# Kernel optimization log

Hardware: AMD Instinct MI355X
Metric: run time of the kernel (lower is better)

Reference implementation:

```python
import jax, jax.numpy as jnp
import numpy as np

N, M, P, C_IN, C_OUT = 100000, 50000, 1600000, 128, 128
NEG_SLOPE = 0.2


def segment_softmax(w, seg, num):
    # numerically-stable softmax of w over segments defined by seg
    m = jax.ops.segment_max(w, seg, num_segments=num)
    e = jnp.exp(w - m[seg])
    s = jax.ops.segment_sum(e, seg, num_segments=num)
    return e / s[seg]


def setup_inputs() -> dict:
    key = jax.random.key(0)
    ks = jax.random.split(key, 8)
    scale = 1.0 / np.sqrt(C_IN)
    return {
        "X": jax.random.normal(ks[0], (N, C_IN), dtype=jnp.float32),
        "pair_v": jax.random.randint(ks[1], (P,), 0, N, dtype=jnp.int32),
        "pair_e": jax.random.randint(ks[2], (P,), 0, M, dtype=jnp.int32),
        "src_v": jax.random.randint(ks[3], (P,), 0, N, dtype=jnp.int32),
        "W_theta": jax.random.normal(ks[4], (C_OUT, C_IN), dtype=jnp.float32) * scale,
        "b_theta": jax.random.normal(ks[5], (C_OUT,), dtype=jnp.float32) * scale,
        "w_src": jax.random.normal(ks[6], (C_OUT,), dtype=jnp.float32) * scale,
        "w_dst": jax.random.normal(ks[7], (C_OUT,), dtype=jnp.float32) * scale,
    }


def reference(X, pair_v, pair_e, src_v, W_theta, b_theta, w_src, w_dst):
    # theta: linear projection (eval mode: dropout = identity, no BN)
    H = X @ W_theta.T + b_theta                      # [N, C_OUT]

    # per-pair attention scores: atten_src(H)[src] + atten_dst(H)[dst]
    s = H @ w_src                                    # [N]
    d = H @ w_dst                                    # [N]
    score = jax.nn.leaky_relu(s[src_v] + d[pair_v], NEG_SLOPE)  # [P]
    score = jnp.clip(score, 0.001, 5.0)

    # degrees
    ones = jnp.ones((P,), dtype=H.dtype)
    de = jnp.maximum(jax.ops.segment_sum(ones, pair_e, num_segments=M), 1.0)  # [M]
    dv = jnp.maximum(jax.ops.segment_sum(ones, pair_v, num_segments=N), 1.0)  # [N]

    dv_isqrt = dv ** -0.5
    Xs = H * dv_isqrt[:, None]
    Xe = jax.ops.segment_sum(Xs[pair_v], pair_e, num_segments=M) / de[:, None]  # [M, C]
    Hs = jax.ops.segment_sum(Xe[pair_e], pair_v, num_segments=N) * dv_isqrt[:, None]

    # v2v(aggr='softmax_then_sum', e2v_weight=score):
    #   v2e softmax_then_sum with unit weights == per-edge mean
    Xe1 = jax.ops.segment_sum(Hs[pair_v], pair_e, num_segments=M) / de[:, None]
    #   e2v: segment-softmax the scores per destination vertex, weighted sum
    alpha = segment_softmax(score, pair_v, N)        # [P]
    Xv1 = jax.ops.segment_sum(alpha[:, None] * Xe1[pair_e], pair_v, num_segments=N)

    # v2v(aggr='mean', v2e_aggr='softmax_then_sum'):
    #   v2e softmax_then_sum with unit weights == per-edge mean; e2v mean
    Xe2 = jax.ops.segment_sum(Xv1[pair_v], pair_e, num_segments=M) / de[:, None]
    Xv2 = jax.ops.segment_sum(Xe2[pair_e], pair_v, num_segments=N) / dv[:, None]

    # is_last=False: ELU activation (dropout identity in eval)
    return jax.nn.elu(Xv2)
```

## Files before the change

kernel.cpp:

```cpp
#include <hip/hip_runtime.h>
#include <math.h>

#define M_EDGES 50000
#define CHUNK 1024

#define NBMAX 200
#define TILE_E 4096
#define TILE_V 4096
#define CAPL_E 44
#define CAPL_V 32

typedef unsigned int u32;
typedef unsigned short u16;
typedef float f32x4 __attribute__((ext_vector_type(4)));
typedef short bf16x8 __attribute__((ext_vector_type(8)));

__device__ __forceinline__ float bflo(u32 u) { return __uint_as_float(u << 16); }
__device__ __forceinline__ float bfhi(u32 u) { return __uint_as_float(u & 0xffff0000u); }
__device__ __forceinline__ u32 packbf(float x, float y) {
  u32 a = __float_as_uint(x); a += 0x7fffu + ((a >> 16) & 1u);
  u32 b = __float_as_uint(y); b += 0x7fffu + ((b >> 16) & 1u);
  return (a >> 16) | (b & 0xffff0000u);
}
__device__ __forceinline__ u32 bf16rne(float x) {
  u32 a = __float_as_uint(x);
  a += 0x7fffu + ((a >> 16) & 1u);
  return a >> 16;
}
__device__ __forceinline__ void bfsplit(float f, u32& h, u32& l) {
  h = bf16rne(f);
  const float hf = __uint_as_float(h << 16);
  l = bf16rne(f - hf);
}

__global__ __launch_bounds__(256) void bin_edge_kernel(
    const int* __restrict__ pair_e, const int* __restrict__ pair_v,
    u32* __restrict__ out, int* __restrict__ gcur,
    int P, int SE, int NB) {
  __shared__ int lcnt[NBMAX];
  __shared__ int gbase[NBMAX];
  __shared__ u32 stage[NBMAX][CAPL_E];
  const int tid = (int)threadIdx.x;
  const int p0 = blockIdx.x * TILE_E;
  const int pend = (p0 + TILE_E < P) ? p0 + TILE_E : P;
  const u32 maskE = (1u << SE) - 1u;
  for (int b = tid; b < NB; b += 256) lcnt[b] = 0;
  __syncthreads();
  for (int p = p0 + tid; p < pend; p += 256) {
    const int e = pair_e[p];
    const int v = pair_v[p];
    const int b = e >> SE;
    const u32 entry = (u32)v | (((u32)e & maskE) << 17);
    const int pos = atomicAdd(&lcnt[b], 1);
    if (pos < CAPL_E) stage[b][pos] = entry;
    else out[atomicAdd(&gcur[b], 1)] = entry;
  }
  __syncthreads();
  for (int b = tid; b < NB; b += 256) {
    const int n = lcnt[b] < CAPL_E ? lcnt[b] : CAPL_E;
    gbase[b] = atomicAdd(&gcur[b], n);
  }
  __syncthreads();
  const int wv = tid >> 6, lane = tid & 63;
  for (int b = wv; b < NB; b += 4) {
    const int n = lcnt[b] < CAPL_E ? lcnt[b] : CAPL_E;
    if (lane < n) out[gbase[b] + lane] = stage[b][lane];
  }
}

__global__ __launch_bounds__(256) void bin_vtx_kernel(
    const int* __restrict__ pair_e, const int* __restrict__ pair_v,
    const int* __restrict__ src_v,
    uint2* __restrict__ out, int* __restrict__ gcur,
    int P, int SV, int NB) {
  __shared__ int lcnt[NBMAX];
  __shared__ int gbase[NBMAX];
  __shared__ uint2 stage[NBMAX][CAPL_V];
  const int tid = (int)threadIdx.x;
  const int p0 = blockIdx.x * TILE_V;
  const int pend = (p0 + TILE_V < P) ? p0 + TILE_V : P;
  const u32 maskV = (1u << SV) - 1u;
  for (int b = tid; b < NB; b += 256) lcnt[b] = 0;
  __syncthreads();
  for (int p = p0 + tid; p < pend; p += 256) {
    const int e = pair_e[p];
    const int v = pair_v[p];
    const int s = src_v[p];
    const int b = v >> SV;
    uint2 entry;
    entry.x = ((u32)v & maskV) | ((u32)e << SV);
    entry.y = (u32)s;
    const int pos = atomicAdd(&lcnt[b], 1);
    if (pos < CAPL_V) stage[b][pos] = entry;
    else out[atomicAdd(&gcur[b], 1)] = entry;
  }
  __syncthreads();
  for (int b = tid; b < NB; b += 256) {
    const int n = lcnt[b] < CAPL_V ? lcnt[b] : CAPL_V;
    gbase[b] = atomicAdd(&gcur[b], n);
  }
  __syncthreads();
  const int wv = tid >> 6, lane = tid & 63;
  for (int b = wv; b < NB; b += 4) {
    const int n = lcnt[b] < CAPL_V ? lcnt[b] : CAPL_V;
    if (lane < n) out[gbase[b] + lane] = stage[b][lane];
  }
}

__global__ void init_gcur_kernel(int* __restrict__ ge, int* __restrict__ gv,
                                 int NBE, int NBV, int capgE, int capgV) {
  const int t = (int)threadIdx.x;
  if (t < NBE) ge[t] = t * capgE;
  if (t < NBV) gv[t] = t * capgV;
}

__global__ __launch_bounds__(256) void bucket_hist_kernel(
    const u32* __restrict__ entE, const int* __restrict__ gcurE, int* __restrict__ cnt_e,
    const uint2* __restrict__ entV, const int* __restrict__ gcurV, int* __restrict__ cnt_v,
    int NBE, int SE, int capgE, int SV, int capgV, int M, int N) {
  __shared__ int h[1024];
  const int b = (int)blockIdx.x;
  const int tid = (int)threadIdx.x;
  if (b < NBE) {
    const int nb = 1 << SE;
    for (int t = tid; t < nb; t += 256) h[t] = 0;
    __syncthreads();
    const int end = gcurE[b];
    for (int i = b * capgE + tid; i < end; i += 256)
      atomicAdd(&h[entE[i] >> 17], 1);
    __syncthreads();
    const int base = b << SE;
    for (int t = tid; t < nb; t += 256)
      if (base + t < M) cnt_e[base + t] = h[t];
  } else {
    const int bb = b - NBE;
    const int nb = 1 << SV;
    for (int t = tid; t < nb; t += 256) h[t] = 0;
    __syncthreads();
    const int end = gcurV[bb];
    const u32 mask = (1u << SV) - 1u;
    for (int i = bb * capgV + tid; i < end; i += 256)
      atomicAdd(&h[entV[i].x & mask], 1);
    __syncthreads();
    const int base = bb << SV;
    for (int t = tid; t < nb; t += 256)
      if (base + t < N) cnt_v[base + t] = h[t];
  }
}

__global__ __launch_bounds__(512) void unbin_edge_kernel(
    const u32* __restrict__ ent, const int* __restrict__ gcur,
    int* __restrict__ cur_e, int* __restrict__ edge_vtx,
    int SE, int capg) {
  const int b = blockIdx.x;
  const int end = gcur[b];
  const int ebase = b << SE;
  for (int i = b * capg + (int)threadIdx.x; i < end; i += 512) {
    const u32 w = ent[i];
    const int v = (int)(w & 0x1ffffu);
    const int e = ebase + (int)(w >> 17);
    edge_vtx[atomicAdd(&cur_e[e], 1)] = v;
  }
}

__global__ __launch_bounds__(512) void unbin_vtx_kernel(
    const uint2* __restrict__ ent, const int* __restrict__ gcur,
    int* __restrict__ cur_v, int2* __restrict__ vtx_es, int* __restrict__ vtx_edge,
    const float* __restrict__ svec, const float* __restrict__ dvec,
    int SV, int capg) {
  const int b = blockIdx.x;
  const int end = gcur[b];
  const int vbase = b << SV;
  const u32 maskV = (1u << SV) - 1u;
  for (int i = b * capg + (int)threadIdx.x; i < end; i += 512) {
    const uint2 w = ent[i];
    const int v = vbase + (int)(w.x & maskV);
    const int e = (int)(w.x >> SV);
    float sc = svec[w.y] + dvec[v];
    sc = sc > 0.f ? sc : 0.2f * sc;
    sc = fminf(fmaxf(sc, 0.001f), 5.0f);
    const int iv = atomicAdd(&cur_v[v], 1);
    vtx_es[iv] = make_int2(e, __float_as_int(__expf(sc)));
    vtx_edge[iv] = e;
  }
}

__global__ __launch_bounds__(1024) void blocksum_kernel(
    const int* __restrict__ cnt_e, const int* __restrict__ cnt_v,
    int* __restrict__ part, int CE, int M, int N) {
  const int b = blockIdx.x;
  const int* cnt;
  int n, chunk;
  if (b < CE) { cnt = cnt_e; n = M; chunk = b; }
  else        { cnt = cnt_v; n = N; chunk = b - CE; }
  const int i = chunk * CHUNK + (int)threadIdx.x;
  int x = (i < n) ? cnt[i] : 0;
#pragma unroll
  for (int m = 32; m >= 1; m >>= 1) x += __shfl_xor(x, m, 64);
  __shared__ int ws[16];
  if ((threadIdx.x & 63) == 0) ws[threadIdx.x >> 6] = x;
  __syncthreads();
  if (threadIdx.x == 0) {
    int t = 0;
#pragma unroll
    for (int q = 0; q < 16; ++q) t += ws[q];
    part[b] = t;
  }
}

__global__ __launch_bounds__(256) void partscan_kernel(
    int* __restrict__ part, int CE, int CV,
    int* __restrict__ off_e, int* __restrict__ off_v, int M, int N) {
  __shared__ int sh[256];
  const int tid = (int)threadIdx.x;
  for (int s = 0; s < 2; ++s) {
    const int base = s ? CE : 0;
    const int count = s ? CV : CE;
    int x = (tid < count) ? part[base + tid] : 0;
    sh[tid] = x;
    __syncthreads();
    for (int ofs = 1; ofs < 256; ofs <<= 1) {
      int v = (tid >= ofs) ? sh[tid - ofs] : 0;
      __syncthreads();
      sh[tid] += v;
      __syncthreads();
    }
    if (tid < count) part[base + tid] = sh[tid] - x;
    if (tid == 0) {
      const int tot = sh[count - 1];
      if (s == 0) off_e[M] = tot; else off_v[N] = tot;
    }
    __syncthreads();
  }
}

__global__ __launch_bounds__(1024) void blockscan_kernel(
    const int* __restrict__ cnt_e, const int* __restrict__ cnt_v,
    const int* __restrict__ part,
    int* __restrict__ off_e, int* __restrict__ off_v,
    int* __restrict__ cur_e, int* __restrict__ cur_v,
    float* __restrict__ de_inv, float* __restrict__ dv_inv, float* __restrict__ dv_isqrt,
    int CE, int M, int N) {
  __shared__ int sh[CHUNK];
  const int b = blockIdx.x;
  const int tid = (int)threadIdx.x;
  const int* cnt;
  int n, chunk;
  int *off, *cur;
  float *i1, *i2;
  if (b < CE) { cnt = cnt_e; n = M; chunk = b;      off = off_e; cur = cur_e; i1 = de_inv; i2 = nullptr; }
  else        { cnt = cnt_v; n = N; chunk = b - CE; off = off_v; cur = cur_v; i1 = dv_inv; i2 = dv_isqrt; }
  const int i = chunk * CHUNK + tid;
  const int x = (i < n) ? cnt[i] : 0;
  sh[tid] = x;
  __syncthreads();
  for (int ofs = 1; ofs < CHUNK; ofs <<= 1) {
    int v = (tid >= ofs) ? sh[tid - ofs] : 0;
    __syncthreads();
    sh[tid] += v;
    __syncthreads();
  }
  if (i < n) {
    const int o = part[b] + sh[tid] - x;
    off[i] = o;
    cur[i] = o;
    const float m = (float)(x > 1 ? x : 1);
    i1[i] = 1.0f / m;
    if (i2) i2[i] = 1.0f / sqrtf(m);
  }
}

__global__ __launch_bounds__(256) void prep_w_kernel(
    const float* __restrict__ W, u16* __restrict__ whi, u16* __restrict__ wlo) {
  const int i = (int)blockIdx.x * 256 + (int)threadIdx.x;
  if (i >= 128 * 128) return;
  u32 h, l;
  bfsplit(W[i], h, l);
  whi[i] = (u16)h;
  wlo[i] = (u16)l;
}

#define XPAD 136
__global__ __launch_bounds__(256) void gemm_mfma_kernel(
    const float* __restrict__ X,
    const u16* __restrict__ whi, const u16* __restrict__ wlo,
    const float* __restrict__ bias, const float* __restrict__ wsrc,
    const float* __restrict__ wdst, const float* __restrict__ dv_isqrt,
    u16* __restrict__ Hb, float* __restrict__ s_out, float* __restrict__ d_out,
    int N) {
  __shared__ u16 xhi[64 * XPAD];
  __shared__ u16 xlo[64 * XPAD];
  __shared__ float sred[64];
  __shared__ float dred[64];
  const int tid = (int)threadIdx.x;
  const int row0 = (int)blockIdx.x * 64;

  if (tid < 64) { sred[tid] = 0.f; dred[tid] = 0.f; }
  for (int g = tid; g < 64 * 32; g += 256) {
    const int r = g >> 5;
    const int k4 = (g & 31) << 2;
    int rr = row0 + r; if (rr >= N) rr = N - 1;
    const float4 v = *(const float4*)(X + (size_t)rr * 128 + k4);
    u32 h0, l0, h1, l1, h2, l2, h3, l3;
    bfsplit(v.x, h0, l0); bfsplit(v.y, h1, l1);
    bfsplit(v.z, h2, l2); bfsplit(v.w, h3, l3);
    *(uint2*)(xhi + r * XPAD + k4) = make_uint2(h0 | (h1 << 16), h2 | (h3 << 16));
    *(uint2*)(xlo + r * XPAD + k4) = make_uint2(l0 | (l1 << 16), l2 | (l3 << 16));
  }
  __syncthreads();

  const int wv = tid >> 6;
  const int l  = tid & 63;
  const int lr = l & 15;
  const int lg = l >> 4;
  const int cb = wv * 32;

  f32x4 zero = {0.f, 0.f, 0.f, 0.f};
  f32x4 acc[4][2];
#pragma unroll
  for (int rt = 0; rt < 4; ++rt) { acc[rt][0] = zero; acc[rt][1] = zero; }

#pragma unroll
  for (int kk = 0; kk < 4; ++kk) {
    const int kof = kk * 32 + lg * 8;
    const bf16x8 bh0 = *(const bf16x8*)(whi + (size_t)(cb + lr) * 128 + kof);
    const bf16x8 bh1 = *(const bf16x8*)(whi + (size_t)(cb + 16 + lr) * 128 + kof);
    const bf16x8 bl0 = *(const bf16x8*)(wlo + (size_t)(cb + lr) * 128 + kof);
    const bf16x8 bl1 = *(const bf16x8*)(wlo + (size_t)(cb + 16 + lr) * 128 + kof);
#pragma unroll
    for (int rt = 0; rt < 4; ++rt) {
      const bf16x8 ah = *(const bf16x8*)(xhi + (rt * 16 + lr) * XPAD + kof);
      const bf16x8 al = *(const bf16x8*)(xlo + (rt * 16 + lr) * XPAD + kof);
      acc[rt][0] = __builtin_amdgcn_mfma_f32_16x16x32_bf16(ah, bh0, acc[rt][0], 0, 0, 0);
      acc[rt][1] = __builtin_amdgcn_mfma_f32_16x16x32_bf16(ah, bh1, acc[rt][1], 0, 0, 0);
      acc[rt][0] = __builtin_amdgcn_mfma_f32_16x16x32_bf16(al, bh0, acc[rt][0], 0, 0, 0);
      acc[rt][1] = __builtin_amdgcn_mfma_f32_16x16x32_bf16(al, bh1, acc[rt][1], 0, 0, 0);
      acc[rt][0] = __builtin_amdgcn_mfma_f32_16x16x32_bf16(ah, bl0, acc[rt][0], 0, 0, 0);
      acc[rt][1] = __builtin_amdgcn_mfma_f32_16x16x32_bf16(ah, bl1, acc[rt][1], 0, 0, 0);
    }
  }

  const int c0 = cb + lr, c1 = cb + 16 + lr;
  const float bb0 = bias[c0], bb1 = bias[c1];
  const float ws0 = wsrc[c0], ws1 = wsrc[c1];
  const float wd0 = wdst[c0], wd1 = wdst[c1];
#pragma unroll
  for (int rt = 0; rt < 4; ++rt) {
#pragma unroll
    for (int j = 0; j < 4; ++j) {
      const int rl = rt * 16 + lg * 4 + j;
      const int row = row0 + rl;
      const float h0 = acc[rt][0][j] + bb0;
      const float h1 = acc[rt][1][j] + bb1;
      float sp = h0 * ws0 + h1 * ws1;
      float dp = h0 * wd0 + h1 * wd1;
#pragma unroll
      for (int m = 1; m <= 8; m <<= 1) {
        sp += __shfl_xor(sp, m, 64);
        dp += __shfl_xor(dp, m, 64);
      }
      if (lr == 0) { atomicAdd(&sred[rl], sp); atomicAdd(&dred[rl], dp); }
      if (row < N) {
        const float sc = dv_isqrt[row];
        Hb[(size_t)row * 128 + c0] = (u16)bf16rne(h0 * sc);
        Hb[(size_t)row * 128 + c1] = (u16)bf16rne(h1 * sc);
      }
    }
  }
  __syncthreads();
  if (tid < 64) {
    const int row = row0 + tid;
    if (row < N) { s_out[row] = sred[tid]; d_out[row] = dred[tid]; }
  }
}

#define ACC8(r, p)                                         \
  a[0] += bflo((r).x) * (p); a[1] += bfhi((r).x) * (p);    \
  a[2] += bflo((r).y) * (p); a[3] += bfhi((r).y) * (p);    \
  a[4] += bflo((r).z) * (p); a[5] += bfhi((r).z) * (p);    \
  a[6] += bflo((r).w) * (p); a[7] += bfhi((r).w) * (p);

__global__ __launch_bounds__(256) void seg_pass_kernel(
    const u16* __restrict__ src, u16* __restrict__ dst,
    const int* __restrict__ off, const int* __restrict__ lst,
    const float* __restrict__ post_scale, int nseg) {
  const int seg = blockIdx.x * 4 + ((int)threadIdx.x >> 6);
  if (seg >= nseg) return;
  const int lane = (int)threadIdx.x & 63;
  const int q = lane >> 4;
  const int cl = lane & 15;
  const int beg = off[seg], end = off[seg + 1];
  const int last = end - 1;
  float a[8] = {};
  for (int t0 = beg + q; t0 < end; t0 += 32) {
    int jj[8];
    float ww[8];
    jj[0] = lst[t0];
    ww[0] = 1.f;
#pragma unroll
    for (int u = 1; u < 8; ++u) {
      const int t = t0 + 4 * u;
      jj[u] = lst[t <= last ? t : last];
      ww[u] = t <= last ? 1.f : 0.f;
    }
    uint4 rr[8];
#pragma unroll
    for (int u = 0; u < 8; ++u)
      rr[u] = *(const uint4*)(src + (size_t)jj[u] * 128 + cl * 8);
#pragma unroll
    for (int u = 0; u < 8; ++u) {
      const uint4 r = rr[u];
      const float p = ww[u];
      ACC8(r, p)
    }
  }
#pragma unroll
  for (int k = 0; k < 8; ++k) {
    a[k] += __shfl_xor(a[k], 16, 64);
    a[k] += __shfl_xor(a[k], 32, 64);
  }
  if (q != 0) return;
  const float ps = post_scale[seg];
  uint4 pk;
  pk.x = packbf(a[0] * ps, a[1] * ps); pk.y = packbf(a[2] * ps, a[3] * ps);
  pk.z = packbf(a[4] * ps, a[5] * ps); pk.w = packbf(a[6] * ps, a[7] * ps);
  *(uint4*)(dst + (size_t)seg * 128 + cl * 8) = pk;
}

__global__ __launch_bounds__(256) void segn_pass_kernel(
    const u16* __restrict__ src, void* __restrict__ dst,
    const int* __restrict__ off, const int* __restrict__ lst,
    const float* __restrict__ post_scale, int nseg, int final_mode) {
  const int seg = blockIdx.x * 4 + ((int)threadIdx.x >> 6);
  if (seg >= nseg) return;
  const int lane = (int)threadIdx.x & 63;
  const int q = lane >> 4;
  const int cl = lane & 15;
  const int beg = off[seg], end = off[seg + 1];
  const int last = end - 1;
  float a[8] = {};
  for (int t0 = beg + q; t0 < end; t0 += 16) {
    const int t1 = t0 + 4, t2 = t0 + 8, t3 = t0 + 12;
    const int j0 = lst[t0];
    const int j1 = lst[t1 <= last ? t1 : last];
    const int j2 = lst[t2 <= last ? t2 : last];
    const int j3 = lst[t3 <= last ? t3 : last];
    const float w1 = t1 <= last ? 1.f : 0.f;
    const float w2 = t2 <= last ? 1.f : 0.f;
    const float w3 = t3 <= last ? 1.f : 0.f;
    const uint4 r0 = *(const uint4*)(src + (size_t)j0 * 128 + cl * 8);
    const uint4 r1 = *(const uint4*)(src + (size_t)j1 * 128 + cl * 8);
    const uint4 r2 = *(const uint4*)(src + (size_t)j2 * 128 + cl * 8);
    const uint4 r3 = *(const uint4*)(src + (size_t)j3 * 128 + cl * 8);
    ACC8(r0, 1.0f) ACC8(r1, w1) ACC8(r2, w2) ACC8(r3, w3)
  }
#pragma unroll
  for (int k = 0; k < 8; ++k) {
    a[k] += __shfl_xor(a[k], 16, 64);
    a[k] += __shfl_xor(a[k], 32, 64);
  }
  if (q != 0) return;
  const float ps = post_scale[seg];
#pragma unroll
  for (int k = 0; k < 8; ++k) a[k] *= ps;
  if (final_mode) {
#pragma unroll
    for (int k = 0; k < 8; ++k) a[k] = a[k] > 0.f ? a[k] : __expf(a[k]) - 1.0f;
    float* o = (float*)dst + (size_t)seg * 128 + cl * 8;
    f32x4 v0 = {a[0], a[1], a[2], a[3]};
    f32x4 v1 = {a[4], a[5], a[6], a[7]};
    __builtin_nontemporal_store(v0, (f32x4*)o);
    __builtin_nontemporal_store(v1, (f32x4*)(o + 4));
  } else {
    uint4 pk;
    pk.x = packbf(a[0], a[1]); pk.y = packbf(a[2], a[3]);
    pk.z = packbf(a[4], a[5]); pk.w = packbf(a[6], a[7]);
    *(uint4*)((u16*)dst + (size_t)seg * 128 + cl * 8) = pk;
  }
}

__global__ __launch_bounds__(256) void attn_pass_kernel(
    const u16* __restrict__ src, u16* __restrict__ dst,
    const int* __restrict__ off, const int2* __restrict__ lst_es, int nseg) {
  const int seg = blockIdx.x * 4 + ((int)threadIdx.x >> 6);
  if (seg >= nseg) return;
  const int lane = (int)threadIdx.x & 63;
  const int q = lane >> 4;
  const int cl = lane & 15;
  const int beg = off[seg], end = off[seg + 1];
  const int last = end - 1;
  float a[8] = {};
  float den = 0.f;
  for (int t0 = beg + q; t0 < end; t0 += 16) {
    const int t1 = t0 + 4, t2 = t0 + 8, t3 = t0 + 12;
    const int2 e0 = lst_es[t0];
    const int2 e1 = lst_es[t1 <= last ? t1 : last];
    const int2 e2 = lst_es[t2 <= last ? t2 : last];
    const int2 e3 = lst_es[t3 <= last ? t3 : last];
    const float s0 = __int_as_float(e0.y);
    const float s1 = t1 <= last ? __int_as_float(e1.y) : 0.f;
    const float s2 = t2 <= last ? __int_as_float(e2.y) : 0.f;
    const float s3 = t3 <= last ? __int_as_float(e3.y) : 0.f;
    const uint4 r0 = *(const uint4*)(src + (size_t)e0.x * 128 + cl * 8);
    const uint4 r1 = *(const uint4*)(src + (size_t)e1.x * 128 + cl * 8);
    const uint4 r2 = *(const uint4*)(src + (size_t)e2.x * 128 + cl * 8);
    const uint4 r3 = *(const uint4*)(src + (size_t)e3.x * 128 + cl * 8);
    ACC8(r0, s0) ACC8(r1, s1) ACC8(r2, s2) ACC8(r3, s3)
    den += s0 + s1 + s2 + s3;
  }
#pragma unroll
  for (int k = 0; k < 8; ++k) {
    a[k] += __shfl_xor(a[k], 16, 64);
    a[k] += __shfl_xor(a[k], 32, 64);
  }
  den += __shfl_xor(den, 16, 64);
  den += __shfl_xor(den, 32, 64);
  const float inv = (end > beg) ? 1.0f / den : 0.0f;
  if (q != 0) return;
  uint4 pk;
  pk.x = packbf(a[0] * inv, a[1] * inv); pk.y = packbf(a[2] * inv, a[3] * inv);
  pk.z = packbf(a[4] * inv, a[5] * inv); pk.w = packbf(a[6] * inv, a[7] * inv);
  *(uint4*)(dst + (size_t)seg * 128 + cl * 8) = pk;
}

extern "C" void kernel_launch(void* const* d_in, const int* in_sizes, int n_in,
                              void* d_out, int out_size, void* d_ws, size_t ws_size,
                              hipStream_t stream) {
  const float* X      = (const float*)d_in[0];
  const int*   pair_v = (const int*)d_in[1];
  const int*   pair_e = (const int*)d_in[2];
  const int*   src_v  = (const int*)d_in[3];
  const float* W      = (const float*)d_in[4];
  const float* bias   = (const float*)d_in[5];
  const float* wsrc   = (const float*)d_in[6];
  const float* wdst   = (const float*)d_in[7];

  const int N = in_sizes[0] / 128;
  const int P = in_sizes[1];
  const int M = M_EDGES;
  const int CE = (M + CHUNK - 1) / CHUNK;
  const int CV = (N + CHUNK - 1) / CHUNK;

  int SE = 8;
  while ((((M - 1) >> SE) + 1) > NBMAX) ++SE;
  const int NBE = ((M - 1) >> SE) + 1;
  int SV = 9;
  while ((((N - 1) >> SV) + 1) > NBMAX) ++SV;
  const int NBV = ((N - 1) >> SV) + 1;
  const int capgE = P / NBE + P / (NBE * 8) + 256;
  const int capgV = P / NBV + P / (NBV * 8) + 256;

  char* w = (char*)d_ws;
  auto alloc = [&](size_t bytes) -> char* {
    char* p = w;
    w += (bytes + 255) & ~(size_t)255;
    return p;
  };
  int*   cnt_e     = (int*)alloc((size_t)M * 4);
  int*   cnt_v     = (int*)alloc((size_t)N * 4);
  int*   cur_e     = (int*)alloc((size_t)M * 4);
  int*   cur_v     = (int*)alloc((size_t)N * 4);
  int*   part      = (int*)alloc((size_t)(CE + CV) * 4);
  int*   edge_off  = (int*)alloc((size_t)(M + 1) * 4);
  int*   vtx_off   = (int*)alloc((size_t)(N + 1) * 4);
  float* de_inv    = (float*)alloc((size_t)M * 4);
  float* dv_inv    = (float*)alloc((size_t)N * 4);
  float* dv_isqrt  = (float*)alloc((size_t)N * 4);
  float* svec      = (float*)alloc((size_t)N * 4);
  float* dvec      = (float*)alloc((size_t)N * 4);
  int*   edge_vtx  = (int*)alloc((size_t)P * 4);
  int2*  vtx_es    = (int2*)alloc((size_t)P * 8);
  int*   vtx_edge  = (int*)alloc((size_t)P * 4);
  u16*   bufN      = (u16*)alloc((size_t)N * 128 * 2);
  u16*   bufM      = (u16*)alloc((size_t)M * 128 * 2);
  u32*   binE      = (u32*)alloc((size_t)NBE * capgE * 4);
  uint2* binV      = (uint2*)alloc((size_t)NBV * capgV * 8);
  int*   gcur_e    = (int*)alloc((size_t)NBE * 4);
  int*   gcur_v    = (int*)alloc((size_t)NBV * 4);
  u16*   whi_g     = (u16*)alloc((size_t)128 * 128 * 2);
  u16*   wlo_g     = (u16*)alloc((size_t)128 * 128 * 2);

  prep_w_kernel<<<64, 256, 0, stream>>>(W, whi_g, wlo_g);
  init_gcur_kernel<<<1, 256, 0, stream>>>(gcur_e, gcur_v, NBE, NBV, capgE, capgV);
  bin_edge_kernel<<<(P + TILE_E - 1) / TILE_E, 256, 0, stream>>>(
      pair_e, pair_v, binE, gcur_e, P, SE, NBE);
  bin_vtx_kernel<<<(P + TILE_V - 1) / TILE_V, 256, 0, stream>>>(
      pair_e, pair_v, src_v, binV, gcur_v, P, SV, NBV);
  bucket_hist_kernel<<<NBE + NBV, 256, 0, stream>>>(
      binE, gcur_e, cnt_e, binV, gcur_v, cnt_v, NBE, SE, capgE, SV, capgV, M, N);
  blocksum_kernel<<<CE + CV, 1024, 0, stream>>>(cnt_e, cnt_v, part, CE, M, N);
  partscan_kernel<<<1, 256, 0, stream>>>(part, CE, CV, edge_off, vtx_off, M, N);
  blockscan_kernel<<<CE + CV, 1024, 0, stream>>>(cnt_e, cnt_v, part, edge_off, vtx_off,
                                                 cur_e, cur_v, de_inv, dv_inv, dv_isqrt,
                                                 CE, M, N);
  gemm_mfma_kernel<<<(N + 63) / 64, 256, 0, stream>>>(X, whi_g, wlo_g, bias, wsrc, wdst,
                                                      dv_isqrt, bufN, svec, dvec, N);
  unbin_edge_kernel<<<NBE, 512, 0, stream>>>(binE, gcur_e, cur_e, edge_vtx, SE, capgE);
  unbin_vtx_kernel<<<NBV, 512, 0, stream>>>(binV, gcur_v, cur_v, vtx_es, vtx_edge,
                                            svec, dvec, SV, capgV);

  const int gm = (M + 3) / 4;
  const int gn = (N + 3) / 4;
  seg_pass_kernel<<<gm, 256, 0, stream>>>(bufN, bufM, edge_off, edge_vtx, de_inv, M);
  segn_pass_kernel<<<gn, 256, 0, stream>>>(bufM, bufN, vtx_off, vtx_edge, dv_isqrt, N, 0);
  seg_pass_kernel<<<gm, 256, 0, stream>>>(bufN, bufM, edge_off, edge_vtx, de_inv, M);
  attn_pass_kernel<<<gn, 256, 0, stream>>>(bufM, bufN, vtx_off, vtx_es, N);
  seg_pass_kernel<<<gm, 256, 0, stream>>>(bufN, bufM, edge_off, edge_vtx, de_inv, M);
  segn_pass_kernel<<<gn, 256, 0, stream>>>(bufM, d_out, vtx_off, vtx_edge, dv_inv, N, 1);
}
```

Baseline: 617.2 us.

## Stage CSR scatter in shared memory with LDS cursors during unbinning

The unbin kernels now keep per-segment write cursors in shared memory and place entries into a shared-memory staging buffer. Each block then writes its contiguous CSR slice to global memory in a coalesced pass. This removes the global atomics on cur_e/cur_v and the random global scatter writes, and drops the cur arrays from the scan kernel. The vertex kernel processes its bin in two halves, so it reads the bin entries twice. Large LDS use (about 38-49KB) limits occupancy, and entries beyond the stage capacity fall back to direct global writes.

```diff
diff --git a/kernel.cpp b/kernel.cpp
--- a/kernel.cpp
+++ b/kernel.cpp
@@ -9,6 +9,8 @@
 #define TILE_V 4096
 #define CAPL_E 44
 #define CAPL_V 32
+#define STAGEE 9472
+#define STAGEV 5888
 
 typedef unsigned int u32;
 typedef unsigned short u16;
@@ -150,38 +152,83 @@
 
 __global__ __launch_bounds__(512) void unbin_edge_kernel(
     const u32* __restrict__ ent, const int* __restrict__ gcur,
-    int* __restrict__ cur_e, int* __restrict__ edge_vtx,
-    int SE, int capg) {
+    const int* __restrict__ off_e, int* __restrict__ edge_vtx,
+    int SE, int capg, int M) {
+  __shared__ int stage[STAGEE];
+  __shared__ int ecur[512];
   const int b = blockIdx.x;
+  const int tid = (int)threadIdx.x;
+  const int ebase = b << SE;
+  const int ne = 1 << SE;
+  const int elim = (ebase + ne < M) ? ebase + ne : M;
+  const int sbeg = off_e[ebase];
+  const int send = off_e[elim];
+  for (int t = tid; t < ne; t += 512)
+    ecur[t] = ((ebase + t) < M ? off_e[ebase + t] : send) - sbeg;
+  __syncthreads();
   const int end = gcur[b];
-  const int ebase = b << SE;
-  for (int i = b * capg + (int)threadIdx.x; i < end; i += 512) {
+  for (int i = b * capg + tid; i < end; i += 512) {
     const u32 w = ent[i];
     const int v = (int)(w & 0x1ffffu);
-    const int e = ebase + (int)(w >> 17);
-    edge_vtx[atomicAdd(&cur_e[e], 1)] = v;
-  }
+    const int le = (int)(w >> 17);
+    const int pos = atomicAdd(&ecur[le], 1);
+    if (pos < STAGEE) stage[pos] = v;
+    else edge_vtx[sbeg + pos] = v;
+  }
+  __syncthreads();
+  const int len = send - sbeg;
+  const int lim = len < STAGEE ? len : STAGEE;
+  for (int i = tid; i < lim; i += 512)
+    edge_vtx[sbeg + i] = stage[i];
 }
 
 __global__ __launch_bounds__(512) void unbin_vtx_kernel(
     const uint2* __restrict__ ent, const int* __restrict__ gcur,
-    int* __restrict__ cur_v, int2* __restrict__ vtx_es, int* __restrict__ vtx_edge,
+    const int* __restrict__ off_v, int2* __restrict__ vtx_es, int* __restrict__ vtx_edge,
     const float* __restrict__ svec, const float* __restrict__ dvec,
-    int SV, int capg) {
+    int SV, int capg, int N) {
+  __shared__ int2 stage[STAGEV];
+  __shared__ int vcur[512];
   const int b = blockIdx.x;
-  const int end = gcur[b];
+  const int tid = (int)threadIdx.x;
   const int vbase = b << SV;
   const u32 maskV = (1u << SV) - 1u;
-  for (int i = b * capg + (int)threadIdx.x; i < end; i += 512) {
-    const uint2 w = ent[i];
-    const int v = vbase + (int)(w.x & maskV);
-    const int e = (int)(w.x >> SV);
-    float sc = svec[w.y] + dvec[v];
-    sc = sc > 0.f ? sc : 0.2f * sc;
-    sc = fminf(fmaxf(sc, 0.001f), 5.0f);
-    const int iv = atomicAdd(&cur_v[v], 1);
-    vtx_es[iv] = make_int2(e, __float_as_int(__expf(sc)));
-    vtx_edge[iv] = e;
+  const int end = gcur[b];
+  const int half = 1 << (SV - 1);
+  for (int s = 0; s < 2; ++s) {
+    const int v0 = vbase + s * half;
+    if (v0 >= N) break;
+    const int vlim = (v0 + half < N) ? v0 + half : N;
+    const int nv = vlim - v0;
+    const int sbeg = off_v[v0];
+    const int send = off_v[vlim];
+    for (int t = tid; t < nv; t += 512)
+      vcur[t] = off_v[v0 + t] - sbeg;
+    __syncthreads();
+    for (int i = b * capg + tid; i < end; i += 512) {
+      const uint2 w = ent[i];
+      const int v = vbase + (int)(w.x & maskV);
+      const u32 lv = (u32)(v - v0);
+      if (lv < (u32)nv) {
+        const int e = (int)(w.x >> SV);
+        float sc = svec[w.y] + dvec[v];
+        sc = sc > 0.f ? sc : 0.2f * sc;
+        sc = fminf(fmaxf(sc, 0.001f), 5.0f);
+        const int2 val = make_int2(e, __float_as_int(__expf(sc)));
+        const int pos = atomicAdd(&vcur[lv], 1);
+        if (pos < STAGEV) stage[pos] = val;
+        else { vtx_es[sbeg + pos] = val; vtx_edge[sbeg + pos] = e; }
+      }
+    }
+    __syncthreads();
+    const int len = send - sbeg;
+    const int lim = len < STAGEV ? len : STAGEV;
+    for (int i = tid; i < lim; i += 512) {
+      const int2 val = stage[i];
+      vtx_es[sbeg + i] = val;
+      vtx_edge[sbeg + i] = val.x;
+    }
+    __syncthreads();
   }
 }
 
@@ -238,7 +285,6 @@
     const int* __restrict__ cnt_e, const int* __restrict__ cnt_v,
     const int* __restrict__ part,
     int* __restrict__ off_e, int* __restrict__ off_v,
-    int* __restrict__ cur_e, int* __restrict__ cur_v,
     float* __restrict__ de_inv, float* __restrict__ dv_inv, float* __restrict__ dv_isqrt,
     int CE, int M, int N) {
   __shared__ int sh[CHUNK];
@@ -246,10 +292,10 @@
   const int tid = (int)threadIdx.x;
   const int* cnt;
   int n, chunk;
-  int *off, *cur;
+  int *off;
   float *i1, *i2;
-  if (b < CE) { cnt = cnt_e; n = M; chunk = b;      off = off_e; cur = cur_e; i1 = de_inv; i2 = nullptr; }
-  else        { cnt = cnt_v; n = N; chunk = b - CE; off = off_v; cur = cur_v; i1 = dv_inv; i2 = dv_isqrt; }
+  if (b < CE) { cnt = cnt_e; n = M; chunk = b;      off = off_e; i1 = de_inv; i2 = nullptr; }
+  else        { cnt = cnt_v; n = N; chunk = b - CE; off = off_v; i1 = dv_inv; i2 = dv_isqrt; }
   const int i = chunk * CHUNK + tid;
   const int x = (i < n) ? cnt[i] : 0;
   sh[tid] = x;
@@ -263,7 +309,6 @@
   if (i < n) {
     const int o = part[b] + sh[tid] - x;
     off[i] = o;
-    cur[i] = o;
     const float m = (float)(x > 1 ? x : 1);
     i1[i] = 1.0f / m;
     if (i2) i2[i] = 1.0f / sqrtf(m);
@@ -558,8 +603,6 @@
   };
   int*   cnt_e     = (int*)alloc((size_t)M * 4);
   int*   cnt_v     = (int*)alloc((size_t)N * 4);
-  int*   cur_e     = (int*)alloc((size_t)M * 4);
-  int*   cur_v     = (int*)alloc((size_t)N * 4);
   int*   part      = (int*)alloc((size_t)(CE + CV) * 4);
   int*   edge_off  = (int*)alloc((size_t)(M + 1) * 4);
   int*   vtx_off   = (int*)alloc((size_t)(N + 1) * 4);
@@ -591,13 +634,13 @@
   blocksum_kernel<<<CE + CV, 1024, 0, stream>>>(cnt_e, cnt_v, part, CE, M, N);
   partscan_kernel<<<1, 256, 0, stream>>>(part, CE, CV, edge_off, vtx_off, M, N);
   blockscan_kernel<<<CE + CV, 1024, 0, stream>>>(cnt_e, cnt_v, part, edge_off, vtx_off,
-                                                 cur_e, cur_v, de_inv, dv_inv, dv_isqrt,
-                                                 CE, M, N);
+                                                 de_inv, dv_inv, dv_isqrt, CE, M, N);
   gemm_mfma_kernel<<<(N + 63) / 64, 256, 0, stream>>>(X, whi_g, wlo_g, bias, wsrc, wdst,
                                                       dv_isqrt, bufN, svec, dvec, N);
-  unbin_edge_kernel<<<NBE, 512, 0, stream>>>(binE, gcur_e, cur_e, edge_vtx, SE, capgE);
-  unbin_vtx_kernel<<<NBV, 512, 0, stream>>>(binV, gcur_v, cur_v, vtx_es, vtx_edge,
-                                            svec, dvec, SV, capgV);
+  unbin_edge_kernel<<<NBE, 512, 0, stream>>>(binE, gcur_e, edge_off, edge_vtx,
+                                             SE, capgE, M);
+  unbin_vtx_kernel<<<NBV, 512, 0, stream>>>(binV, gcur_v, vtx_off, vtx_es, vtx_edge,
+                                            svec, dvec, SV, capgV, N);
 
   const int gm = (M + 3) / 4;
   const int gn = (N + 3) / 4;
```

Measured after the change: 566.0 us. -8.3%, faster.
